# Kernel optimization log

Hardware: AMD Instinct MI355X
Metric: run time of the kernel (lower is better)

The kernel has to match this reference:

```python
import jax, jax.numpy as jnp
import numpy as np
import math

B, S, DQ, DK, DV, H = 8, 2048, 256, 256, 256, 4
DH = DV // H
EPS = 1e-5

def _layernorm(x, g, b):
    mu = jnp.mean(x, axis=-1, keepdims=True)
    var = jnp.mean(jnp.square(x - mu), axis=-1, keepdims=True)
    return (x - mu) * jax.lax.rsqrt(var + EPS) * g + b

def setup_inputs() -> dict:
    key = jax.random.key(0)
    ks = jax.random.split(key, 12)
    s_in = 1.0 / math.sqrt(DQ)
    s_v = 1.0 / math.sqrt(DV)
    return {
        "Q": jax.random.normal(ks[0], (B, S, DQ), dtype=jnp.float32),
        "K": jax.random.normal(ks[1], (B, S, DK), dtype=jnp.float32),
        "Wq": jax.random.uniform(ks[2], (DQ, DV), jnp.float32, -s_in, s_in),
        "bq": jax.random.uniform(ks[3], (DV,), jnp.float32, -s_in, s_in),
        "Wk": jax.random.uniform(ks[4], (DK, DV), jnp.float32, -s_in, s_in),
        "bk": jax.random.uniform(ks[5], (DV,), jnp.float32, -s_in, s_in),
        "Wv": jax.random.uniform(ks[6], (DK, DV), jnp.float32, -s_in, s_in),
        "bv": jax.random.uniform(ks[7], (DV,), jnp.float32, -s_in, s_in),
        "Wo": jax.random.uniform(ks[8], (DV, DV), jnp.float32, -s_v, s_v),
        "bo": jax.random.uniform(ks[9], (DV,), jnp.float32, -s_v, s_v),
        "g0": jnp.ones((DV,), jnp.float32),
        "beta0": jnp.zeros((DV,), jnp.float32),
        "g1": jnp.ones((DV,), jnp.float32),
        "beta1": jnp.zeros((DV,), jnp.float32),
    }

def reference(Q, K, Wq, bq, Wk, bk, Wv, bv, Wo, bo, g0, beta0, g1, beta1):
    q = Q @ Wq + bq                    # [B,S,DV]
    k = K @ Wk + bk
    v = K @ Wv + bv
    q4 = q.reshape(B, S, H, DH)
    k4 = k.reshape(B, S, H, DH)
    v4 = v.reshape(B, S, H, DH)
    scores = jnp.einsum('bqhd,bkhd->bhqk', q4, k4) / math.sqrt(DH)
    A = jax.nn.softmax(scores, axis=-1)
    o = q4 + jnp.einsum('bhqk,bkhd->bqhd', A, v4)  # residual with projected Q per head
    O = o.reshape(B, S, DV)
    O = _layernorm(O, g0, beta0)
    O = O + jax.nn.relu(O @ Wo + bo)
    O = _layernorm(O, g1, beta1)
    return O
```

## Files before the change

kernel.cpp:

```cpp
#include <hip/hip_runtime.h>
#include <hip/hip_bf16.h>
#include <stdint.h>

typedef uint16_t u16;
typedef uint32_t u32;
typedef __attribute__((ext_vector_type(8))) short short8;
typedef __attribute__((ext_vector_type(4))) float f32x4;

#define LOG2E 1.44269504088896340736f

__device__ __forceinline__ u16 f2bf(float f) {
    u32 u = __builtin_bit_cast(u32, f);
    return (u16)((u + 0x7fffu + ((u >> 16) & 1u)) >> 16);
}
__device__ __forceinline__ float bf2f(u16 h) {
    u32 u = ((u32)h) << 16;
    return __builtin_bit_cast(float, u);
}

__global__ __launch_bounds__(256)
void cvt2_kernel(const float* __restrict__ Q, const float* __restrict__ K,
                 u16* __restrict__ Qc, u16* __restrict__ Kc) {
    const int bid = blockIdx.x;
    const float* src = (bid < 2048) ? Q : K;
    u16* dst = (bid < 2048) ? Qc : Kc;
    const size_t i = ((size_t)(bid & 2047) * 256 + threadIdx.x) * 8;
    float4 a = *(const float4*)(src + i);
    float4 b = *(const float4*)(src + i + 4);
    uint4 o;
    o.x = (u32)f2bf(a.x) | ((u32)f2bf(a.y) << 16);
    o.y = (u32)f2bf(a.z) | ((u32)f2bf(a.w) << 16);
    o.z = (u32)f2bf(b.x) | ((u32)f2bf(b.y) << 16);
    o.w = (u32)f2bf(b.z) | ((u32)f2bf(b.w) << 16);
    *(uint4*)(dst + i) = o;
}

__global__ void wt_kernel(const float* __restrict__ Wq, const float* __restrict__ Wk,
                          const float* __restrict__ Wv, const float* __restrict__ Wo,
                          const float* __restrict__ bk, u16* __restrict__ WT,
                          float* __restrict__ bks) {
    const int wsel = blockIdx.y, k = blockIdx.x, n = threadIdx.x;
    const float* W = (wsel == 0) ? Wq : (wsel == 1) ? Wk : (wsel == 2) ? Wv : Wo;
    const float scale = (wsel == 1) ? (0.125f * LOG2E) : 1.0f;
    WT[(size_t)wsel * 65536 + (size_t)n * 256 + k] = f2bf(W[(size_t)k * 256 + n] * scale);
    if (wsel == 1 && k == 0) bks[n] = bk[n] * (0.125f * LOG2E);
}

template<int EPI>
__device__ __forceinline__ void gemm_body(const u16* __restrict__ A, const u16* __restrict__ BT,
                                          const float* __restrict__ bias, const float* resid,
                                          void* outp) {
    __shared__ u16 As[128 * 64];
    __shared__ u16 Bs[128 * 64];
    const int tid = threadIdx.x;
    const int w = tid >> 6, lane = tid & 63;
    const int g = lane >> 4, lo = lane & 15;
    const int rowB = blockIdx.x * 128;
    const int colB = blockIdx.y * 128;
    const int wr = (w >> 1) * 64, wc = (w & 1) * 64;

    const f32x4 fz = {0.f, 0.f, 0.f, 0.f};
    f32x4 acc[4][4];
#pragma unroll
    for (int m = 0; m < 4; ++m)
#pragma unroll
        for (int n = 0; n < 4; ++n) acc[m][n] = fz;

    const int srow = tid & 127;
    const int shalf = tid >> 7;

#pragma unroll 1
    for (int kt = 0; kt < 4; ++kt) {
        const int k0 = kt * 64;
        __syncthreads();
        {
            const u16* ga = A + (size_t)(rowB + srow) * 256 + k0 + shalf * 32;
            uint4 a0 = *(const uint4*)ga;
            uint4 a1 = *(const uint4*)(ga + 8);
            uint4 a2 = *(const uint4*)(ga + 16);
            uint4 a3 = *(const uint4*)(ga + 24);
            const u16* gb = BT + (size_t)(colB + srow) * 256 + k0 + shalf * 32;
            uint4 b0 = *(const uint4*)gb;
            uint4 b1 = *(const uint4*)(gb + 8);
            uint4 b2 = *(const uint4*)(gb + 16);
            uint4 b3 = *(const uint4*)(gb + 24);
            const u32 sw = (u32)((srow & 7) << 4);
            const u32 ba = (u32)(srow * 128 + shalf * 64);
            *(uint4*)((char*)As + ((ba) ^ sw))      = a0;
            *(uint4*)((char*)As + ((ba + 16) ^ sw)) = a1;
            *(uint4*)((char*)As + ((ba + 32) ^ sw)) = a2;
            *(uint4*)((char*)As + ((ba + 48) ^ sw)) = a3;
            *(uint4*)((char*)Bs + ((ba) ^ sw))      = b0;
            *(uint4*)((char*)Bs + ((ba + 16) ^ sw)) = b1;
            *(uint4*)((char*)Bs + ((ba + 32) ^ sw)) = b2;
            *(uint4*)((char*)Bs + ((ba + 48) ^ sw)) = b3;
        }
        __syncthreads();
#pragma unroll
        for (int c = 0; c < 2; ++c) {
            short8 af[4], bfr[4];
#pragma unroll
            for (int m = 0; m < 4; ++m) {
                const int row = wr + m * 16 + lo;
                const u32 addr = (u32)(row * 128 + c * 64 + g * 16) ^ (u32)((row & 7) << 4);
                af[m] = *(const short8*)((char*)As + addr);
            }
#pragma unroll
            for (int n = 0; n < 4; ++n) {
                const int row = wc + n * 16 + lo;
                const u32 addr = (u32)(row * 128 + c * 64 + g * 16) ^ (u32)((row & 7) << 4);
                bfr[n] = *(const short8*)((char*)Bs + addr);
            }
#pragma unroll
            for (int m = 0; m < 4; ++m)
#pragma unroll
                for (int n = 0; n < 4; ++n)
                    acc[m][n] = __builtin_amdgcn_mfma_f32_16x16x32_bf16(af[m], bfr[n], acc[m][n], 0, 0, 0);
        }
    }

    float bv[4];
#pragma unroll
    for (int n = 0; n < 4; ++n) bv[n] = bias[colB + wc + n * 16 + lo];

    if (EPI == 0) {
        u16* out = (u16*)outp;
#pragma unroll
        for (int m = 0; m < 4; ++m)
#pragma unroll
            for (int r = 0; r < 4; ++r) {
                const size_t row = (size_t)(rowB + wr + m * 16 + g * 4 + r);
#pragma unroll
                for (int n = 0; n < 4; ++n)
                    out[row * 256 + colB + wc + n * 16 + lo] = f2bf(acc[m][n][r] + bv[n]);
            }
    } else {
        float* out = (float*)outp;
#pragma unroll
        for (int m = 0; m < 4; ++m)
#pragma unroll
            for (int r = 0; r < 4; ++r) {
                const size_t row = (size_t)(rowB + wr + m * 16 + g * 4 + r);
#pragma unroll
                for (int n = 0; n < 4; ++n) {
                    const size_t idx = row * 256 + colB + wc + n * 16 + lo;
                    out[idx] = resid[idx] + fmaxf(acc[m][n][r] + bv[n], 0.f);
                }
            }
    }
}

__global__ __launch_bounds__(256)
void proj_kernel(const u16* __restrict__ Qc, const u16* __restrict__ Kc,
                 const u16* __restrict__ WT, const float* __restrict__ bq,
                 const float* __restrict__ bks, const float* __restrict__ bvv,
                 u16* __restrict__ qb, u16* __restrict__ kbuf, u16* __restrict__ vbuf) {
    const int z = blockIdx.z;
    const u16* A = (z == 0) ? Qc : Kc;
    const u16* BT = WT + z * 65536;
    const float* bias = (z == 0) ? bq : (z == 1) ? bks : bvv;
    u16* out = (z == 0) ? qb : (z == 1) ? kbuf : vbuf;
    gemm_body<0>(A, BT, bias, nullptr, (void*)out);
}

__global__ __launch_bounds__(256)
void mlp_kernel(const u16* __restrict__ A, const u16* __restrict__ BT,
                const float* __restrict__ bias, const float* resid, float* outp) {
    gemm_body<1>(A, BT, bias, resid, (void*)outp);
}

__global__ __launch_bounds__(512, 4)
void attn_kernel(const u16* __restrict__ qb, const u16* __restrict__ kb,
                 const u16* __restrict__ vb, float* __restrict__ Obuf) {
    __shared__ u16 Klds[2 * 64 * 64];
    __shared__ u16 Vtlds[2 * 64 * 64];
    __shared__ u16 Plds[8 * 16 * 64];
    const int tid = threadIdx.x;
    const int w = tid >> 6, lane = tid & 63;
    const int g = lane >> 4, lo = lane & 15;
    const int q0 = blockIdx.x * 128;
    const int h = blockIdx.y, b = blockIdx.z;
    const size_t hbase = (size_t)b * 2048 * 256 + (size_t)h * 64;

    short8 qf[2];
#pragma unroll
    for (int c = 0; c < 2; ++c) {
        const size_t row = (size_t)(q0 + w * 16 + lo);
        qf[c] = *(const short8*)&qb[hbase + row * 256 + c * 32 + g * 8];
    }

    const f32x4 fz = {0.f, 0.f, 0.f, 0.f};
    f32x4 oacc[4];
#pragma unroll
    for (int n = 0; n < 4; ++n) oacc[n] = fz;
    float m_run = -1e30f;
    float l_run = 0.f;

    char* Pb = (char*)Plds + w * 2048;

    const bool kRole = (tid < 256);
    const int skey = tid & 63, sseg = (tid >> 6) & 3;
    const int t4 = tid & 255;
    const int vkey = (t4 & 31) * 2, vd0 = (t4 >> 5) * 8;
    const u16* gbase;
    int goff2;
    if (kRole) { gbase = &kb[hbase + (size_t)skey * 256 + sseg * 16]; goff2 = 8; }
    else       { gbase = &vb[hbase + (size_t)vkey * 256 + vd0];       goff2 = 256; }

    uint4 s0, s1;
    auto load_tile = [&](int kt) {
        const u16* p = gbase + (size_t)kt * 16384;
        s0 = *(const uint4*)p;
        s1 = *(const uint4*)(p + goff2);
    };
    auto write_tile = [&](int sel) {
        if (kRole) {
            char* Kb_ = (char*)Klds + sel * 8192;
            const u32 sw = (u32)((skey & 7) << 4);
            const u32 ba = (u32)(skey * 128 + sseg * 32);
            *(uint4*)(Kb_ + ((ba) ^ sw)) = s0;
            *(uint4*)(Kb_ + ((ba + 16) ^ sw)) = s1;
        } else {
            char* Vb_ = (char*)Vtlds + sel * 8192;
            union { uint4 v; u16 hh[8]; } a0, a1;
            a0.v = s0; a1.v = s1;
#pragma unroll
            for (int i = 0; i < 8; ++i) {
                const int d = vd0 + i;
                const u32 addr = (u32)(d * 128 + vkey * 2) ^ (u32)((d & 7) << 4);
                *(u32*)(Vb_ + addr) = (u32)a0.hh[i] | ((u32)a1.hh[i] << 16);
            }
        }
    };

    load_tile(0);
    write_tile(0);
    load_tile(1);
    __syncthreads();

#pragma unroll 1
    for (int kt = 0; kt < 32; ++kt) {
        const int cur = kt & 1;
        char* Klb = (char*)Klds + cur * 8192;
        char* Vtb = (char*)Vtlds + cur * 8192;

        f32x4 sc[4];
#pragma unroll
        for (int km = 0; km < 4; ++km) sc[km] = fz;
#pragma unroll
        for (int c = 0; c < 2; ++c)
#pragma unroll
            for (int km = 0; km < 4; ++km) {
                const int key = km * 16 + lo;
                const u32 addr = (u32)(key * 128 + c * 64 + g * 16) ^ (u32)((key & 7) << 4);
                const short8 kf = *(const short8*)(Klb + addr);
                sc[km] = __builtin_amdgcn_mfma_f32_16x16x32_bf16(kf, qf[c], sc[km], 0, 0, 0);
            }

        float mt = -1e30f;
#pragma unroll
        for (int km = 0; km < 4; ++km)
#pragma unroll
            for (int r = 0; r < 4; ++r) mt = fmaxf(mt, sc[km][r]);
        mt = fmaxf(mt, __shfl_xor(mt, 16));
        mt = fmaxf(mt, __shfl_xor(mt, 32));
        if (!__all(mt <= m_run + 11.5f)) {
            const float mnew = fmaxf(m_run, mt);
            const float alpha = __builtin_amdgcn_exp2f(m_run - mnew);
            l_run *= alpha;
#pragma unroll
            for (int r = 0; r < 4; ++r) {
                const float a = __shfl(alpha, (lane & 48) | (g * 4 + r));
#pragma unroll
                for (int n = 0; n < 4; ++n) oacc[n][r] *= a;
            }
            m_run = mnew;
        }
        float ls = 0.f;
#pragma unroll
        for (int km = 0; km < 4; ++km)
#pragma unroll
            for (int r = 0; r < 4; ++r) {
                const float p = __builtin_amdgcn_exp2f(sc[km][r] - m_run);
                sc[km][r] = p;
                ls += p;
            }
        ls += __shfl_xor(ls, 16);
        ls += __shfl_xor(ls, 32);
        l_run += ls;

        {
            const u32 sw = (u32)((lo & 7) << 4);
#pragma unroll
            for (int km = 0; km < 4; ++km) {
                uint2 val;
                val.x = (u32)f2bf(sc[km][0]) | ((u32)f2bf(sc[km][1]) << 16);
                val.y = (u32)f2bf(sc[km][2]) | ((u32)f2bf(sc[km][3]) << 16);
                const u32 addr = (u32)(lo * 128 + km * 32 + g * 8) ^ sw;
                *(uint2*)(Pb + addr) = val;
            }
        }

#pragma unroll
        for (int c = 0; c < 2; ++c) {
            const u32 paddr = (u32)(lo * 128 + c * 64 + g * 16) ^ (u32)((lo & 7) << 4);
            const short8 pf = *(const short8*)(Pb + paddr);
#pragma unroll
            for (int n = 0; n < 4; ++n) {
                const int d = n * 16 + lo;
                const u32 addr = (u32)(d * 128 + c * 64 + g * 16) ^ (u32)((d & 7) << 4);
                const short8 vf = *(const short8*)(Vtb + addr);
                oacc[n] = __builtin_amdgcn_mfma_f32_16x16x32_bf16(pf, vf, oacc[n], 0, 0, 0);
            }
        }

        if (kt < 31) write_tile(cur ^ 1);
        if (kt < 30) load_tile(kt + 2);
        __syncthreads();
    }

#pragma unroll
    for (int r = 0; r < 4; ++r) {
        const float li = 1.0f / __shfl(l_run, (lane & 48) | (g * 4 + r));
        const size_t row = (size_t)(q0 + w * 16 + g * 4 + r);
#pragma unroll
        for (int n = 0; n < 4; ++n) {
            const int d = n * 16 + lo;
            const size_t idx = hbase + row * 256 + d;
            Obuf[idx] = oacc[n][r] * li + bf2f(qb[idx]);
        }
    }
}

template<bool WB>
__global__ __launch_bounds__(256)
void ln_kernel(const float* in, const float* __restrict__ gam,
               const float* __restrict__ bet, float* of,
               u16* __restrict__ ob) {
    const int w = threadIdx.x >> 6, lane = threadIdx.x & 63;
    const size_t row = (size_t)blockIdx.x * 4 + w;
    const float4 v = ((const float4*)(in + row * 256))[lane];
    float s = v.x + v.y + v.z + v.w;
    float q = v.x * v.x + v.y * v.y + v.z * v.z + v.w * v.w;
#pragma unroll
    for (int m = 1; m <= 32; m <<= 1) {
        s += __shfl_xor(s, m);
        q += __shfl_xor(q, m);
    }
    const float mu = s * (1.f / 256.f);
    const float var = q * (1.f / 256.f) - mu * mu;
    const float rstd = rsqrtf(var + 1e-5f);
    const float4 gv = ((const float4*)gam)[lane];
    const float4 bv = ((const float4*)bet)[lane];
    float4 y;
    y.x = (v.x - mu) * rstd * gv.x + bv.x;
    y.y = (v.y - mu) * rstd * gv.y + bv.y;
    y.z = (v.z - mu) * rstd * gv.z + bv.z;
    y.w = (v.w - mu) * rstd * gv.w + bv.w;
    ((float4*)(of + row * 256))[lane] = y;
    if (WB) {
        uint2 pk;
        pk.x = (u32)f2bf(y.x) | ((u32)f2bf(y.y) << 16);
        pk.y = (u32)f2bf(y.z) | ((u32)f2bf(y.w) << 16);
        *(uint2*)(ob + row * 256 + lane * 4) = pk;
    }
}

extern "C" void kernel_launch(void* const* d_in, const int* in_sizes, int n_in,
                              void* d_out, int out_size, void* d_ws, size_t ws_size,
                              hipStream_t stream) {
    const float* Q  = (const float*)d_in[0];
    const float* K  = (const float*)d_in[1];
    const float* Wq = (const float*)d_in[2];
    const float* bq = (const float*)d_in[3];
    const float* Wk = (const float*)d_in[4];
    const float* bk = (const float*)d_in[5];
    const float* Wv = (const float*)d_in[6];
    const float* bv = (const float*)d_in[7];
    const float* Wo = (const float*)d_in[8];
    const float* bo = (const float*)d_in[9];
    const float* g0 = (const float*)d_in[10];
    const float* be0 = (const float*)d_in[11];
    const float* g1 = (const float*)d_in[12];
    const float* be1 = (const float*)d_in[13];
    float* out = (float*)d_out;

    const size_t NE = (size_t)8 * 2048 * 256;
    char* ws = (char*)d_ws;
    size_t off = 0;
    auto alloc = [&](size_t bytes) { char* p = ws + off; off += (bytes + 255) & ~(size_t)255; return p; };
    u16* Qc   = (u16*)alloc(NE * 2);
    u16* Kc   = (u16*)alloc(NE * 2);
    u16* qb   = (u16*)alloc(NE * 2);
    u16* kbuf = (u16*)alloc(NE * 2);
    u16* vbuf = (u16*)alloc(NE * 2);
    u16* WT   = (u16*)alloc(4 * 65536 * 2);
    float* bks = (float*)alloc(256 * 4);
    u16* Xb   = Qc;
    float* Obuf = out;

    cvt2_kernel<<<4096, 256, 0, stream>>>(Q, K, Qc, Kc);
    wt_kernel<<<dim3(256, 4), 256, 0, stream>>>(Wq, Wk, Wv, Wo, bk, WT, bks);

    proj_kernel<<<dim3(128, 2, 3), 256, 0, stream>>>(Qc, Kc, WT, bq, bks, bv, qb, kbuf, vbuf);

    attn_kernel<<<dim3(16, 4, 8), 512, 0, stream>>>(qb, kbuf, vbuf, Obuf);

    ln_kernel<true><<<4096, 256, 0, stream>>>(Obuf, g0, be0, Obuf, Xb);
    mlp_kernel<<<dim3(128, 2), 256, 0, stream>>>(Xb, WT + 3 * 65536, bo, Obuf, Obuf);
    ln_kernel<false><<<4096, 256, 0, stream>>>(Obuf, g1, be1, out, nullptr);
}
```

Measured before the change: 134.4 us.

## Shrink attention blocks to 64 queries, compute row sums via MFMA, merge prep kernels

Attention blocks drop from 512 to 256 threads, each covering 64 queries, and every thread now loads both K and V tiles instead of splitting them by role. The grid doubles, which changes occupancy and spreads work across more blocks. The softmax row sum moves from per-thread exp sums plus cross-lane shuffles to an extra MFMA of P against a vector of bf16 ones. This sums the bf16-rounded P that is actually multiplied with V, at the cost of one more MFMA per tile. The Q/K conversion and weight-transpose kernels are merged into a single launch to save one kernel launch.

```diff
diff --git a/kernel.cpp b/kernel.cpp
--- a/kernel.cpp
+++ b/kernel.cpp
@@ -17,33 +17,38 @@
     u32 u = ((u32)h) << 16;
     return __builtin_bit_cast(float, u);
 }
+__device__ __forceinline__ u32 pack_bf16(float lo, float hi) {
+    return (u32)f2bf(lo) | ((u32)f2bf(hi) << 16);
+}
 
 __global__ __launch_bounds__(256)
-void cvt2_kernel(const float* __restrict__ Q, const float* __restrict__ K,
-                 u16* __restrict__ Qc, u16* __restrict__ Kc) {
+void prep_kernel(const float* __restrict__ Q, const float* __restrict__ K,
+                 u16* __restrict__ Qc, u16* __restrict__ Kc,
+                 const float* __restrict__ Wq, const float* __restrict__ Wk,
+                 const float* __restrict__ Wv, const float* __restrict__ Wo,
+                 const float* __restrict__ bk, u16* __restrict__ WT,
+                 float* __restrict__ bks) {
     const int bid = blockIdx.x;
-    const float* src = (bid < 2048) ? Q : K;
-    u16* dst = (bid < 2048) ? Qc : Kc;
-    const size_t i = ((size_t)(bid & 2047) * 256 + threadIdx.x) * 8;
-    float4 a = *(const float4*)(src + i);
-    float4 b = *(const float4*)(src + i + 4);
-    uint4 o;
-    o.x = (u32)f2bf(a.x) | ((u32)f2bf(a.y) << 16);
-    o.y = (u32)f2bf(a.z) | ((u32)f2bf(a.w) << 16);
-    o.z = (u32)f2bf(b.x) | ((u32)f2bf(b.y) << 16);
-    o.w = (u32)f2bf(b.z) | ((u32)f2bf(b.w) << 16);
-    *(uint4*)(dst + i) = o;
-}
-
-__global__ void wt_kernel(const float* __restrict__ Wq, const float* __restrict__ Wk,
-                          const float* __restrict__ Wv, const float* __restrict__ Wo,
-                          const float* __restrict__ bk, u16* __restrict__ WT,
-                          float* __restrict__ bks) {
-    const int wsel = blockIdx.y, k = blockIdx.x, n = threadIdx.x;
-    const float* W = (wsel == 0) ? Wq : (wsel == 1) ? Wk : (wsel == 2) ? Wv : Wo;
-    const float scale = (wsel == 1) ? (0.125f * LOG2E) : 1.0f;
-    WT[(size_t)wsel * 65536 + (size_t)n * 256 + k] = f2bf(W[(size_t)k * 256 + n] * scale);
-    if (wsel == 1 && k == 0) bks[n] = bk[n] * (0.125f * LOG2E);
+    if (bid < 4096) {
+        const float* src = (bid < 2048) ? Q : K;
+        u16* dst = (bid < 2048) ? Qc : Kc;
+        const size_t i = ((size_t)(bid & 2047) * 256 + threadIdx.x) * 8;
+        float4 a = *(const float4*)(src + i);
+        float4 b = *(const float4*)(src + i + 4);
+        uint4 o;
+        o.x = pack_bf16(a.x, a.y);
+        o.y = pack_bf16(a.z, a.w);
+        o.z = pack_bf16(b.x, b.y);
+        o.w = pack_bf16(b.z, b.w);
+        *(uint4*)(dst + i) = o;
+    } else {
+        const int idx = bid - 4096;
+        const int wsel = idx >> 8, k = idx & 255, n = threadIdx.x;
+        const float* W = (wsel == 0) ? Wq : (wsel == 1) ? Wk : (wsel == 2) ? Wv : Wo;
+        const float scale = (wsel == 1) ? (0.125f * LOG2E) : 1.0f;
+        WT[(size_t)wsel * 65536 + (size_t)n * 256 + k] = f2bf(W[(size_t)k * 256 + n] * scale);
+        if (wsel == 1 && k == 0) bks[n] = bk[n] * (0.125f * LOG2E);
+    }
 }
 
 template<int EPI>
@@ -169,16 +174,16 @@
     gemm_body<1>(A, BT, bias, resid, (void*)outp);
 }
 
-__global__ __launch_bounds__(512, 4)
+__global__ __launch_bounds__(256, 4)
 void attn_kernel(const u16* __restrict__ qb, const u16* __restrict__ kb,
                  const u16* __restrict__ vb, float* __restrict__ Obuf) {
     __shared__ u16 Klds[2 * 64 * 64];
     __shared__ u16 Vtlds[2 * 64 * 64];
-    __shared__ u16 Plds[8 * 16 * 64];
+    __shared__ u16 Plds[4 * 16 * 64];
     const int tid = threadIdx.x;
     const int w = tid >> 6, lane = tid & 63;
     const int g = lane >> 4, lo = lane & 15;
-    const int q0 = blockIdx.x * 128;
+    const int q0 = blockIdx.x * 64;
     const int h = blockIdx.y, b = blockIdx.z;
     const size_t hbase = (size_t)b * 2048 * 256 + (size_t)h * 64;
 
@@ -188,48 +193,45 @@
         const size_t row = (size_t)(q0 + w * 16 + lo);
         qf[c] = *(const short8*)&qb[hbase + row * 256 + c * 32 + g * 8];
     }
+    const short8 vones = {0x3F80, 0x3F80, 0x3F80, 0x3F80, 0x3F80, 0x3F80, 0x3F80, 0x3F80};
 
     const f32x4 fz = {0.f, 0.f, 0.f, 0.f};
     f32x4 oacc[4];
 #pragma unroll
     for (int n = 0; n < 4; ++n) oacc[n] = fz;
+    f32x4 l_acc = fz;
     float m_run = -1e30f;
-    float l_run = 0.f;
 
     char* Pb = (char*)Plds + w * 2048;
 
-    const bool kRole = (tid < 256);
-    const int skey = tid & 63, sseg = (tid >> 6) & 3;
-    const int t4 = tid & 255;
-    const int vkey = (t4 & 31) * 2, vd0 = (t4 >> 5) * 8;
-    const u16* gbase;
-    int goff2;
-    if (kRole) { gbase = &kb[hbase + (size_t)skey * 256 + sseg * 16]; goff2 = 8; }
-    else       { gbase = &vb[hbase + (size_t)vkey * 256 + vd0];       goff2 = 256; }
-
-    uint4 s0, s1;
+    const int skey = tid & 63, sseg = tid >> 6;
+    const int vkey = (tid & 31) * 2, vd0 = (tid >> 5) * 8;
+    const u16* gk = &kb[hbase + (size_t)skey * 256 + sseg * 16];
+    const u16* gv = &vb[hbase + (size_t)vkey * 256 + vd0];
+
+    uint4 k0s, k1s, v0s, v1s;
     auto load_tile = [&](int kt) {
-        const u16* p = gbase + (size_t)kt * 16384;
-        s0 = *(const uint4*)p;
-        s1 = *(const uint4*)(p + goff2);
+        const u16* pk = gk + (size_t)kt * 16384;
+        k0s = *(const uint4*)pk;
+        k1s = *(const uint4*)(pk + 8);
+        const u16* pv = gv + (size_t)kt * 16384;
+        v0s = *(const uint4*)pv;
+        v1s = *(const uint4*)(pv + 256);
     };
     auto write_tile = [&](int sel) {
-        if (kRole) {
-            char* Kb_ = (char*)Klds + sel * 8192;
-            const u32 sw = (u32)((skey & 7) << 4);
-            const u32 ba = (u32)(skey * 128 + sseg * 32);
-            *(uint4*)(Kb_ + ((ba) ^ sw)) = s0;
-            *(uint4*)(Kb_ + ((ba + 16) ^ sw)) = s1;
-        } else {
-            char* Vb_ = (char*)Vtlds + sel * 8192;
-            union { uint4 v; u16 hh[8]; } a0, a1;
-            a0.v = s0; a1.v = s1;
-#pragma unroll
-            for (int i = 0; i < 8; ++i) {
-                const int d = vd0 + i;
-                const u32 addr = (u32)(d * 128 + vkey * 2) ^ (u32)((d & 7) << 4);
-                *(u32*)(Vb_ + addr) = (u32)a0.hh[i] | ((u32)a1.hh[i] << 16);
-            }
+        char* Kb_ = (char*)Klds + sel * 8192;
+        const u32 sw = (u32)((skey & 7) << 4);
+        const u32 ba = (u32)(skey * 128 + sseg * 32);
+        *(uint4*)(Kb_ + ((ba) ^ sw)) = k0s;
+        *(uint4*)(Kb_ + ((ba + 16) ^ sw)) = k1s;
+        char* Vb_ = (char*)Vtlds + sel * 8192;
+        union { uint4 v; u16 hh[8]; } a0, a1;
+        a0.v = v0s; a1.v = v1s;
+#pragma unroll
+        for (int i = 0; i < 8; ++i) {
+            const int d = vd0 + i;
+            const u32 addr = (u32)(d * 128 + vkey * 2) ^ (u32)((d & 7) << 4);
+            *(u32*)(Vb_ + addr) = (u32)a0.hh[i] | ((u32)a1.hh[i] << 16);
         }
     };
 
@@ -267,35 +269,28 @@
         if (!__all(mt <= m_run + 11.5f)) {
             const float mnew = fmaxf(m_run, mt);
             const float alpha = __builtin_amdgcn_exp2f(m_run - mnew);
-            l_run *= alpha;
 #pragma unroll
             for (int r = 0; r < 4; ++r) {
                 const float a = __shfl(alpha, (lane & 48) | (g * 4 + r));
+                l_acc[r] *= a;
 #pragma unroll
                 for (int n = 0; n < 4; ++n) oacc[n][r] *= a;
             }
             m_run = mnew;
         }
-        float ls = 0.f;
 #pragma unroll
         for (int km = 0; km < 4; ++km)
 #pragma unroll
-            for (int r = 0; r < 4; ++r) {
-                const float p = __builtin_amdgcn_exp2f(sc[km][r] - m_run);
-                sc[km][r] = p;
-                ls += p;
-            }
-        ls += __shfl_xor(ls, 16);
-        ls += __shfl_xor(ls, 32);
-        l_run += ls;
+            for (int r = 0; r < 4; ++r)
+                sc[km][r] = __builtin_amdgcn_exp2f(sc[km][r] - m_run);
 
         {
             const u32 sw = (u32)((lo & 7) << 4);
 #pragma unroll
             for (int km = 0; km < 4; ++km) {
                 uint2 val;
-                val.x = (u32)f2bf(sc[km][0]) | ((u32)f2bf(sc[km][1]) << 16);
-                val.y = (u32)f2bf(sc[km][2]) | ((u32)f2bf(sc[km][3]) << 16);
+                val.x = pack_bf16(sc[km][0], sc[km][1]);
+                val.y = pack_bf16(sc[km][2], sc[km][3]);
                 const u32 addr = (u32)(lo * 128 + km * 32 + g * 8) ^ sw;
                 *(uint2*)(Pb + addr) = val;
             }
@@ -312,6 +307,7 @@
                 const short8 vf = *(const short8*)(Vtb + addr);
                 oacc[n] = __builtin_amdgcn_mfma_f32_16x16x32_bf16(pf, vf, oacc[n], 0, 0, 0);
             }
+            l_acc = __builtin_amdgcn_mfma_f32_16x16x32_bf16(pf, vones, l_acc, 0, 0, 0);
         }
 
         if (kt < 31) write_tile(cur ^ 1);
@@ -321,7 +317,7 @@
 
 #pragma unroll
     for (int r = 0; r < 4; ++r) {
-        const float li = 1.0f / __shfl(l_run, (lane & 48) | (g * 4 + r));
+        const float li = 1.0f / l_acc[r];
         const size_t row = (size_t)(q0 + w * 16 + g * 4 + r);
 #pragma unroll
         for (int n = 0; n < 4; ++n) {
@@ -360,8 +356,8 @@
     ((float4*)(of + row * 256))[lane] = y;
     if (WB) {
         uint2 pk;
-        pk.x = (u32)f2bf(y.x) | ((u32)f2bf(y.y) << 16);
-        pk.y = (u32)f2bf(y.z) | ((u32)f2bf(y.w) << 16);
+        pk.x = pack_bf16(y.x, y.y);
+        pk.y = pack_bf16(y.z, y.w);
         *(uint2*)(ob + row * 256 + lane * 4) = pk;
     }
 }
@@ -399,12 +395,11 @@
     u16* Xb   = Qc;
     float* Obuf = out;
 
-    cvt2_kernel<<<4096, 256, 0, stream>>>(Q, K, Qc, Kc);
-    wt_kernel<<<dim3(256, 4), 256, 0, stream>>>(Wq, Wk, Wv, Wo, bk, WT, bks);
+    prep_kernel<<<5120, 256, 0, stream>>>(Q, K, Qc, Kc, Wq, Wk, Wv, Wo, bk, WT, bks);
 
     proj_kernel<<<dim3(128, 2, 3), 256, 0, stream>>>(Qc, Kc, WT, bq, bks, bv, qb, kbuf, vbuf);
 
-    attn_kernel<<<dim3(16, 4, 8), 512, 0, stream>>>(qb, kbuf, vbuf, Obuf);
+    attn_kernel<<<dim3(32, 4, 8), 256, 0, stream>>>(qb, kbuf, vbuf, Obuf);
 
     ln_kernel<true><<<4096, 256, 0, stream>>>(Obuf, g0, be0, Obuf, Xb);
     mlp_kernel<<<dim3(128, 2), 256, 0, stream>>>(Xb, WT + 3 * 65536, bo, Obuf, Obuf);
```

Result: slower. 148.4 us (+10.4%).
